# Kernel tuning notes

Hardware: AMD Instinct MI355X
Metric: run time of the kernel (lower is better)

Reference implementation:

```python
import jax, jax.numpy as jnp
import numpy as np

NUM_HEADS = 16
HEAD_DIM = 64
WINDOW = 512
D_MODEL = NUM_HEADS * HEAD_DIM
BATCH = 2
SEQ = 2048


def setup_inputs() -> dict:
    key = jax.random.key(0)
    k1, k2, k3 = jax.random.split(key, 3)
    x = jax.random.normal(k1, (BATCH, SEQ, D_MODEL), dtype=jnp.float32)
    # Dense layer params (lecun_normal-like scale for stability)
    qkv_kernel = jax.random.normal(k2, (D_MODEL, 3 * NUM_HEADS * HEAD_DIM), dtype=jnp.float32) / np.sqrt(D_MODEL)
    qkv_bias = jnp.zeros((3 * NUM_HEADS * HEAD_DIM,), dtype=jnp.float32)
    out_kernel = jax.random.normal(k3, (NUM_HEADS * HEAD_DIM, D_MODEL), dtype=jnp.float32) / np.sqrt(D_MODEL)
    out_bias = jnp.zeros((D_MODEL,), dtype=jnp.float32)
    return {"x": x, "qkv_kernel": qkv_kernel, "qkv_bias": qkv_bias,
            "out_kernel": out_kernel, "out_bias": out_bias}


def reference(x, qkv_kernel, qkv_bias, out_kernel, out_bias):
    b, s, d = x.shape
    qkv = x @ qkv_kernel + qkv_bias                       # (b, s, 3*H*hd)
    qkv = qkv.reshape(b, s, 3, NUM_HEADS, HEAD_DIM)
    q = qkv[:, :, 0].transpose(0, 2, 1, 3)                # (b, H, s, hd)
    k = qkv[:, :, 1].transpose(0, 2, 1, 3)
    v = qkv[:, :, 2].transpose(0, 2, 1, 3)
    scale = 1.0 / jnp.sqrt(jnp.float32(HEAD_DIM)).astype(x.dtype)
    scores = jnp.einsum('bhqd,bhkd->bhqk', q, k) * scale  # (b, H, s, s)
    rows = jnp.arange(s)[:, None]
    cols = jnp.arange(s)[None, :]
    window_mask = (rows - cols >= 0) & (rows - cols < WINDOW)
    scores = jnp.where(window_mask[None, None], scores, jnp.asarray(-1e9, scores.dtype))
    attn = jax.nn.softmax(scores, axis=-1)
    out = jnp.einsum('bhqk,bhkd->bhqd', attn, v)          # (b, H, s, hd)
    out = out.transpose(0, 2, 1, 3).reshape(b, s, -1)
    return out @ out_kernel + out_bias
```

## Files before the change

kernel.cpp:

```cpp
#include <hip/hip_runtime.h>
#include <cstdint>
#include <cstddef>

#define NUM_HEADS 16
#define HEAD_DIM  64
#define WINDOW    512
#define D_MODEL   1024
#define BATCH     2
#define SEQ       2048
#define MTOT      (BATCH*SEQ)
#define NQKV      (3*D_MODEL)

typedef short bf16x8 __attribute__((ext_vector_type(8)));
typedef float f32x4  __attribute__((ext_vector_type(4)));

__device__ __forceinline__ f32x4 mfma16(bf16x8 a, bf16x8 b, f32x4 c) {
  return __builtin_amdgcn_mfma_f32_16x16x32_bf16(a, b, c, 0, 0, 0);
}

__device__ __forceinline__ unsigned short f2bf(float f) {
  unsigned int u = __float_as_uint(f);
  u += 0x7fffu + ((u >> 16) & 1u);
  return (unsigned short)(u >> 16);
}
__device__ __forceinline__ float bf2f(unsigned short b) {
  return __uint_as_float(((unsigned int)b) << 16);
}

__device__ __forceinline__ void gld16(const unsigned short* g, unsigned short* l) {
  __builtin_amdgcn_global_load_lds(
      (const __attribute__((address_space(1))) unsigned int*)g,
      (__attribute__((address_space(3))) unsigned int*)l, 16, 0, 0);
}

__global__ __launch_bounds__(256) void prep_kernel(const float* __restrict__ x,
                                                   const float* __restrict__ qkv_w,
                                                   const float* __restrict__ out_w,
                                                   unsigned short* __restrict__ Xb,
                                                   unsigned short* __restrict__ Wq,
                                                   unsigned short* __restrict__ Wo) {
  __shared__ float tile[32][33];
  const int bid = blockIdx.x, t = threadIdx.x;
  if (bid < 4096) {
    int i = (bid * 256 + t) * 4;
    float4 v = *(const float4*)(x + i);
    ushort4 o;
    o.x = f2bf(v.x); o.y = f2bf(v.y); o.z = f2bf(v.z); o.w = f2bf(v.w);
    *(ushort4*)(Xb + i) = o;
    return;
  }
  const float* in; unsigned short* out; int R, C, bx, by;
  if (bid < 7168) { int b2 = bid - 4096; in = qkv_w; out = Wq; R = D_MODEL; C = NQKV; bx = b2 % 96; by = b2 / 96; }
  else            { int b2 = bid - 7168; in = out_w; out = Wo; R = D_MODEL; C = D_MODEL; bx = b2 & 31; by = b2 >> 5; }
  int tx = t & 31, ty = t >> 5;
  int c0 = bx * 32, r0 = by * 32;
#pragma unroll
  for (int i = 0; i < 32; i += 8)
    tile[ty + i][tx] = in[(size_t)(r0 + ty + i) * C + c0 + tx];
  __syncthreads();
#pragma unroll
  for (int i = 0; i < 32; i += 8)
    out[(size_t)(c0 + ty + i) * R + r0 + tx] = f2bf(tile[tx][ty + i]);
}

template<int TI, bool SWAP, int K>
__device__ __forceinline__ void gemm_mainloop_p3(const unsigned short* __restrict__ A,
                                                 const unsigned short* __restrict__ Bt,
                                                 int m0, int n0,
                                                 unsigned short* sA, unsigned short* sB,
                                                 f32x4 (&acc)[TI][4]) {
  const int t = threadIdx.x;
  const int lane = t & 63, wave = t >> 6;
  const int wm = wave >> 1, wn = wave & 1;
  const int lhi = lane >> 4, llo = lane & 15;
  f32x4 zero = {0.f, 0.f, 0.f, 0.f};
#pragma unroll
  for (int i = 0; i < TI; ++i)
#pragma unroll
    for (int j = 0; j < 4; ++j) acc[i][j] = zero;

  const int cswz = (((t & 3) ^ ((t >> 3) & 3)) << 3);
  const unsigned short* gA = A  + (size_t)(m0 + (t >> 2)) * K + cswz;
  const unsigned short* gB = Bt + (size_t)(n0 + (t >> 2)) * K + cswz;
  const size_t rowskip = (size_t)64 * K;
  const int ldsT = t * 8;
  const int rsw  = (lhi ^ ((llo >> 1) & 3)) * 8;
  const int aoff = (wm * (TI * 16) + llo) * 32 + rsw;
  const int boff = (wn * 64 + llo) * 32 + rsw;
  constexpr int ABUF = TI * 1024;
  constexpr int nIter = K / 32;

  auto stage = [&](int it2) {
    unsigned short* dA = sA + (it2 % 3) * ABUF;
    unsigned short* dB = sB + (it2 % 3) * 4096;
    const int kk = it2 * 32;
    gld16(gA + kk, dA + ldsT);
    if (TI == 4) gld16(gA + kk + rowskip, dA + ldsT + 2048);
    gld16(gB + kk, dB + ldsT);
    gld16(gB + kk + rowskip, dB + ldsT + 2048);
  };

  stage(0);
  stage(1);
#pragma unroll
  for (int it = 0; it < nIter; ++it) {
    if (it + 1 < nIter) {
      if (TI == 4) asm volatile("s_waitcnt vmcnt(4)\n\ts_barrier" ::: "memory");
      else         asm volatile("s_waitcnt vmcnt(3)\n\ts_barrier" ::: "memory");
    } else {
      asm volatile("s_waitcnt vmcnt(0)\n\ts_barrier" ::: "memory");
    }
    if (it + 2 < nIter) stage(it + 2);
    const unsigned short* cA = sA + (it % 3) * ABUF;
    const unsigned short* cB = sB + (it % 3) * 4096;
    bf16x8 af[TI], bfr[4];
#pragma unroll
    for (int i = 0; i < TI; ++i) af[i]  = *(const bf16x8*)(cA + aoff + i * 512);
#pragma unroll
    for (int j = 0; j < 4; ++j)  bfr[j] = *(const bf16x8*)(cB + boff + j * 512);
#pragma unroll
    for (int i = 0; i < TI; ++i)
#pragma unroll
      for (int j = 0; j < 4; ++j)
        acc[i][j] = SWAP ? mfma16(bfr[j], af[i], acc[i][j])
                         : mfma16(af[i], bfr[j], acc[i][j]);
  }
}

__global__ __launch_bounds__(256) void qkv_gemm_kernel(const unsigned short* __restrict__ Xb,
                                                       const unsigned short* __restrict__ Wt,
                                                       const float* __restrict__ bias,
                                                       unsigned short* __restrict__ Qw,
                                                       unsigned short* __restrict__ Kw,
                                                       unsigned short* __restrict__ Vtw) {
  __shared__ __align__(16) unsigned short sA[3][128 * 32];
  __shared__ __align__(16) unsigned short sB[3][128 * 32];
  f32x4 acc[4][4];
  const int m0 = blockIdx.y * 128, n0 = blockIdx.x * 128;
  const int t = threadIdx.x, lane = t & 63, wave = t >> 6;
  const int wm = wave >> 1, wn = wave & 1, lhi = lane >> 4, llo = lane & 15;

  if (n0 < 2048) {
    gemm_mainloop_p3<4, false, D_MODEL>(Xb, Wt, m0, n0, sA[0], sB[0], acc);
    const int c = n0 >> 10;
    unsigned short* __restrict__ Dst = (c == 0) ? Qw : Kw;
    const float qscale = (c == 0) ? 0.125f : 1.0f;
#pragma unroll
    for (int ti = 0; ti < 4; ++ti) {
#pragma unroll
      for (int tj = 0; tj < 4; ++tj) {
        int n = n0 + wn * 64 + tj * 16 + llo;
        float bv = bias[n];
        int h = (n >> 6) & 15, d = n & 63;
#pragma unroll
        for (int r = 0; r < 4; ++r) {
          int m = m0 + wm * 64 + ti * 16 + lhi * 4 + r;
          int b = m >> 11, s = m & 2047;
          int bh = b * 16 + h;
          Dst[((size_t)(bh * 2048 + s)) * 64 + d] = f2bf((acc[ti][tj][r] + bv) * qscale);
        }
      }
    }
  } else {
    gemm_mainloop_p3<4, true, D_MODEL>(Xb, Wt, m0, n0, sA[0], sB[0], acc);
#pragma unroll
    for (int ti = 0; ti < 4; ++ti) {
      int m = m0 + wm * 64 + ti * 16 + llo;
      int b = m >> 11, s = m & 2047;
#pragma unroll
      for (int tj = 0; tj < 4; ++tj) {
        int nb = n0 + wn * 64 + tj * 16 + lhi * 4;
        float4 bv = *(const float4*)(bias + nb);
        int h = (nb >> 6) & 15, dbase = nb & 63;
        int bh = b * 16 + h;
        float bvr[4] = {bv.x, bv.y, bv.z, bv.w};
#pragma unroll
        for (int r = 0; r < 4; ++r)
          Vtw[(size_t)(bh * 64 + dbase + r) * 2048 + s] = f2bf(acc[ti][tj][r] + bvr[r]);
      }
    }
  }
}

__global__ __launch_bounds__(512) void attn_kernel(const unsigned short* __restrict__ Qw,
                                                   const unsigned short* __restrict__ Kw,
                                                   const unsigned short* __restrict__ Vtw,
                                                   unsigned short* __restrict__ AO) {
  __shared__ __align__(16) unsigned short sK[3][64 * 64];
  __shared__ __align__(16) unsigned short sV[3][64 * 64];
  __shared__ __align__(16) unsigned short sP[8][16 * 72];
  const int t = threadIdx.x, lane = t & 63, wave = t >> 6;
  const int lhi = lane >> 4, llo = lane & 15;
  const int bh = blockIdx.x;
  const int q0 = (15 - blockIdx.y) << 7;
  const unsigned short* Qb = Qw  + (size_t)bh * 2048 * 64;
  const unsigned short* Kb = Kw  + (size_t)bh * 2048 * 64;
  const unsigned short* Vb = Vtw + (size_t)bh * 64 * 2048;

  const int qw = q0 + wave * 16;
  const int qrow = qw + llo;
  bf16x8 qf0 = *(const bf16x8*)(Qb + (size_t)qrow * 64 + lhi * 8);
  bf16x8 qf1 = *(const bf16x8*)(Qb + (size_t)qrow * 64 + 32 + lhi * 8);

  const int srow = t >> 3;
  const int scol = ((t & 7) ^ (srow & 7)) * 8;
  const int cpos  = (lhi ^ (llo & 7)) * 8;
  const int cposx = cpos ^ 32;

  float m_i = -1e30f, l_i = 0.f;
  f32x4 o[4];
  f32x4 zero = {0.f, 0.f, 0.f, 0.f};
#pragma unroll
  for (int td = 0; td < 4; ++td) o[td] = zero;

  const int kt_lo = (q0 > 511) ? ((q0 - 511) >> 6) : 0;
  const int kt_hi = (q0 + 127) >> 6;

  auto stageKV = [&](int j) {
    const int k0 = j << 6;
    unsigned short* dK = sK[j % 3];
    unsigned short* dV = sV[j % 3];
    gld16(Kb + (size_t)(k0 + srow) * 64 + scol, dK + t * 8);
    gld16(Vb + (size_t)srow * 2048 + k0 + scol, dV + t * 8);
  };

  stageKV(kt_lo);
  stageKV(kt_lo + 1);

  for (int kt = kt_lo; kt <= kt_hi; ++kt) {
    if (kt < kt_hi) asm volatile("s_waitcnt vmcnt(2)\n\ts_barrier" ::: "memory");
    else            asm volatile("s_waitcnt vmcnt(0)\n\ts_barrier" ::: "memory");
    if (kt + 2 <= kt_hi) stageKV(kt + 2);
    const int k0 = kt << 6;
    if (k0 > qw + 15 || k0 + 63 < qw - (WINDOW - 1)) continue;

    const unsigned short* bK = sK[kt % 3];
    const unsigned short* bV = sV[kt % 3];

    f32x4 st[4];
#pragma unroll
    for (int tk = 0; tk < 4; ++tk) {
      const unsigned short* kr = bK + (tk * 16 + llo) * 64;
      bf16x8 kf0 = *(const bf16x8*)(kr + cpos);
      bf16x8 kf1 = *(const bf16x8*)(kr + cposx);
      f32x4 z = zero;
      z = mfma16(kf0, qf0, z);
      z = mfma16(kf1, qf1, z);
      st[tk] = z;
    }

    const int kb = k0 + lhi * 4;
    float mx = -1e30f;
#pragma unroll
    for (int tk = 0; tk < 4; ++tk)
#pragma unroll
      for (int r = 0; r < 4; ++r) {
        int key = kb + tk * 16 + r;
        bool ok = (key <= qrow) && (qrow - key < WINDOW);
        float s = ok ? st[tk][r] : -1e30f;
        st[tk][r] = s;
        mx = fmaxf(mx, s);
      }
    mx = fmaxf(mx, __shfl_xor(mx, 16));
    mx = fmaxf(mx, __shfl_xor(mx, 32));
    float mn = fmaxf(m_i, mx);
    float a  = __expf(m_i - mn);
    float rs = 0.f;
    unsigned short* pw = &sP[wave][llo * 72];
#pragma unroll
    for (int tk = 0; tk < 4; ++tk) {
      ushort4 pb;
      pb.x = f2bf(__expf(st[tk][0] - mn));
      pb.y = f2bf(__expf(st[tk][1] - mn));
      pb.z = f2bf(__expf(st[tk][2] - mn));
      pb.w = f2bf(__expf(st[tk][3] - mn));
      *(ushort4*)(pw + tk * 16 + lhi * 4) = pb;
      rs += bf2f(pb.x) + bf2f(pb.y) + bf2f(pb.z) + bf2f(pb.w);
    }
    rs += __shfl_xor(rs, 16);
    rs += __shfl_xor(rs, 32);
    l_i = l_i * a + rs;
    m_i = mn;

    float aR[4];
#pragma unroll
    for (int r = 0; r < 4; ++r) aR[r] = __shfl(a, lhi * 4 + r);
#pragma unroll
    for (int td = 0; td < 4; ++td)
#pragma unroll
      for (int r = 0; r < 4; ++r) o[td][r] *= aR[r];

    bf16x8 pf0 = *(const bf16x8*)(pw + lhi * 8);
    bf16x8 pf1 = *(const bf16x8*)(pw + 32 + lhi * 8);
#pragma unroll
    for (int td = 0; td < 4; ++td) {
      const unsigned short* vr = bV + (td * 16 + llo) * 64;
      bf16x8 vf0 = *(const bf16x8*)(vr + cpos);
      bf16x8 vf1 = *(const bf16x8*)(vr + cposx);
      o[td] = mfma16(pf0, vf0, o[td]);
      o[td] = mfma16(pf1, vf1, o[td]);
    }
  }

  float lR[4];
#pragma unroll
  for (int r = 0; r < 4; ++r) lR[r] = 1.f / __shfl(l_i, lhi * 4 + r);
  const int b = bh >> 4, h = bh & 15;
#pragma unroll
  for (int td = 0; td < 4; ++td)
#pragma unroll
    for (int r = 0; r < 4; ++r) {
      int qr = q0 + wave * 16 + lhi * 4 + r;
      AO[(size_t)(b * 2048 + qr) * 1024 + h * 64 + td * 16 + llo] = f2bf(o[td][r] * lR[r]);
    }
}

__global__ __launch_bounds__(256) void out_gemm_kernel(const unsigned short* __restrict__ AO,
                                                       const unsigned short* __restrict__ Wt,
                                                       const float* __restrict__ bias,
                                                       float* __restrict__ out) {
  __shared__ __align__(16) unsigned short sA[3][128 * 32];
  __shared__ __align__(16) unsigned short sB[3][128 * 32];
  f32x4 acc[4][4];
  const int m0 = blockIdx.y * 128, n0 = blockIdx.x * 128;
  gemm_mainloop_p3<4, false, D_MODEL>(AO, Wt, m0, n0, sA[0], sB[0], acc);

  const int t = threadIdx.x, lane = t & 63, wave = t >> 6;
  const int wm = wave >> 1, wn = wave & 1, lhi = lane >> 4, llo = lane & 15;
#pragma unroll
  for (int ti = 0; ti < 4; ++ti)
#pragma unroll
    for (int tj = 0; tj < 4; ++tj) {
      int n = n0 + wn * 64 + tj * 16 + llo;
      float bv = bias[n];
#pragma unroll
      for (int r = 0; r < 4; ++r) {
        int m = m0 + wm * 64 + ti * 16 + lhi * 4 + r;
        out[(size_t)m * D_MODEL + n] = acc[ti][tj][r] + bv;
      }
    }
}

extern "C" void kernel_launch(void* const* d_in, const int* in_sizes, int n_in,
                              void* d_out, int out_size, void* d_ws, size_t ws_size,
                              hipStream_t stream) {
  const float* x      = (const float*)d_in[0];
  const float* qkv_w  = (const float*)d_in[1];
  const float* qkv_b  = (const float*)d_in[2];
  const float* out_w  = (const float*)d_in[3];
  const float* out_b  = (const float*)d_in[4];
  float* out = (float*)d_out;
  char* ws = (char*)d_ws;

  unsigned short* Xb  = (unsigned short*)(ws);
  unsigned short* Wq  = (unsigned short*)(ws + ((size_t)8  << 20));
  unsigned short* Wo  = (unsigned short*)(ws + ((size_t)14 << 20));
  unsigned short* Qw  = (unsigned short*)(ws + ((size_t)16 << 20));
  unsigned short* Kw  = (unsigned short*)(ws + ((size_t)24 << 20));
  unsigned short* Vtw = (unsigned short*)(ws + ((size_t)32 << 20));
  unsigned short* AO  = (unsigned short*)(ws + ((size_t)40 << 20));

  prep_kernel<<<8192, 256, 0, stream>>>(x, qkv_w, out_w, Xb, Wq, Wo);
  qkv_gemm_kernel<<<dim3(NQKV / 128, MTOT / 128), 256, 0, stream>>>(Xb, Wq, qkv_b, Qw, Kw, Vtw);
  attn_kernel<<<dim3(BATCH * NUM_HEADS, SEQ / 128), 512, 0, stream>>>(Qw, Kw, Vtw, AO);
  out_gemm_kernel<<<dim3(D_MODEL / 128, MTOT / 128), 256, 0, stream>>>(AO, Wo, out_b, out);
}
```

Before: 169.8 us.

## Use 512-thread GEMM blocks with 8 waves and skip masking on interior attention tiles

Both GEMM kernels now run 512 threads (8 waves) per 128x128 tile. Each wave computes a 32x64 sub-tile, which halves the accumulator registers and lets every thread issue one load per operand per stage. This is meant to raise occupancy and latency hiding, at the cost of fewer MFMAs per LDS fragment load. The attention kernel also gains a fast path that skips per-element window-mask checks when a key tile lies entirely inside the window for all rows of the wave.

```diff
diff --git a/kernel.cpp b/kernel.cpp
--- a/kernel.cpp
+++ b/kernel.cpp
@@ -63,63 +63,54 @@
     out[(size_t)(c0 + ty + i) * R + r0 + tx] = f2bf(tile[tx][ty + i]);
 }
 
-template<int TI, bool SWAP, int K>
-__device__ __forceinline__ void gemm_mainloop_p3(const unsigned short* __restrict__ A,
+template<bool SWAP, int K>
+__device__ __forceinline__ void gemm_mainloop512(const unsigned short* __restrict__ A,
                                                  const unsigned short* __restrict__ Bt,
                                                  int m0, int n0,
                                                  unsigned short* sA, unsigned short* sB,
-                                                 f32x4 (&acc)[TI][4]) {
+                                                 f32x4 (&acc)[2][4]) {
   const int t = threadIdx.x;
   const int lane = t & 63, wave = t >> 6;
-  const int wm = wave >> 1, wn = wave & 1;
+  const int wr = wave >> 1, wc = wave & 1;
   const int lhi = lane >> 4, llo = lane & 15;
   f32x4 zero = {0.f, 0.f, 0.f, 0.f};
 #pragma unroll
-  for (int i = 0; i < TI; ++i)
+  for (int i = 0; i < 2; ++i)
 #pragma unroll
     for (int j = 0; j < 4; ++j) acc[i][j] = zero;
 
   const int cswz = (((t & 3) ^ ((t >> 3) & 3)) << 3);
   const unsigned short* gA = A  + (size_t)(m0 + (t >> 2)) * K + cswz;
   const unsigned short* gB = Bt + (size_t)(n0 + (t >> 2)) * K + cswz;
-  const size_t rowskip = (size_t)64 * K;
   const int ldsT = t * 8;
   const int rsw  = (lhi ^ ((llo >> 1) & 3)) * 8;
-  const int aoff = (wm * (TI * 16) + llo) * 32 + rsw;
-  const int boff = (wn * 64 + llo) * 32 + rsw;
-  constexpr int ABUF = TI * 1024;
+  const int aoff = (wr * 32 + llo) * 32 + rsw;
+  const int boff = (wc * 64 + llo) * 32 + rsw;
   constexpr int nIter = K / 32;
 
-  auto stage = [&](int it2) {
-    unsigned short* dA = sA + (it2 % 3) * ABUF;
-    unsigned short* dB = sB + (it2 % 3) * 4096;
-    const int kk = it2 * 32;
-    gld16(gA + kk, dA + ldsT);
-    if (TI == 4) gld16(gA + kk + rowskip, dA + ldsT + 2048);
-    gld16(gB + kk, dB + ldsT);
-    gld16(gB + kk + rowskip, dB + ldsT + 2048);
+  auto stage = [&](int s) {
+    unsigned short* dA = sA + (s % 3) * 4096;
+    unsigned short* dB = sB + (s % 3) * 4096;
+    gld16(gA + s * 32, dA + ldsT);
+    gld16(gB + s * 32, dB + ldsT);
   };
 
   stage(0);
   stage(1);
 #pragma unroll
   for (int it = 0; it < nIter; ++it) {
-    if (it + 1 < nIter) {
-      if (TI == 4) asm volatile("s_waitcnt vmcnt(4)\n\ts_barrier" ::: "memory");
-      else         asm volatile("s_waitcnt vmcnt(3)\n\ts_barrier" ::: "memory");
-    } else {
-      asm volatile("s_waitcnt vmcnt(0)\n\ts_barrier" ::: "memory");
-    }
+    if (it + 1 < nIter) asm volatile("s_waitcnt vmcnt(2)\n\ts_barrier" ::: "memory");
+    else                asm volatile("s_waitcnt vmcnt(0)\n\ts_barrier" ::: "memory");
     if (it + 2 < nIter) stage(it + 2);
-    const unsigned short* cA = sA + (it % 3) * ABUF;
+    const unsigned short* cA = sA + (it % 3) * 4096;
     const unsigned short* cB = sB + (it % 3) * 4096;
-    bf16x8 af[TI], bfr[4];
-#pragma unroll
-    for (int i = 0; i < TI; ++i) af[i]  = *(const bf16x8*)(cA + aoff + i * 512);
+    bf16x8 af[2], bfr[4];
+#pragma unroll
+    for (int i = 0; i < 2; ++i) af[i]  = *(const bf16x8*)(cA + aoff + i * 512);
 #pragma unroll
     for (int j = 0; j < 4; ++j)  bfr[j] = *(const bf16x8*)(cB + boff + j * 512);
 #pragma unroll
-    for (int i = 0; i < TI; ++i)
+    for (int i = 0; i < 2; ++i)
 #pragma unroll
       for (int j = 0; j < 4; ++j)
         acc[i][j] = SWAP ? mfma16(bfr[j], af[i], acc[i][j])
@@ -127,49 +118,49 @@
   }
 }
 
-__global__ __launch_bounds__(256) void qkv_gemm_kernel(const unsigned short* __restrict__ Xb,
-                                                       const unsigned short* __restrict__ Wt,
-                                                       const float* __restrict__ bias,
-                                                       unsigned short* __restrict__ Qw,
-                                                       unsigned short* __restrict__ Kw,
-                                                       unsigned short* __restrict__ Vtw) {
+__global__ __launch_bounds__(512, 6) void qkv_gemm_kernel(const unsigned short* __restrict__ Xb,
+                                                          const unsigned short* __restrict__ Wt,
+                                                          const float* __restrict__ bias,
+                                                          unsigned short* __restrict__ Qw,
+                                                          unsigned short* __restrict__ Kw,
+                                                          unsigned short* __restrict__ Vtw) {
   __shared__ __align__(16) unsigned short sA[3][128 * 32];
   __shared__ __align__(16) unsigned short sB[3][128 * 32];
-  f32x4 acc[4][4];
+  f32x4 acc[2][4];
   const int m0 = blockIdx.y * 128, n0 = blockIdx.x * 128;
   const int t = threadIdx.x, lane = t & 63, wave = t >> 6;
-  const int wm = wave >> 1, wn = wave & 1, lhi = lane >> 4, llo = lane & 15;
+  const int wr = wave >> 1, wc = wave & 1, lhi = lane >> 4, llo = lane & 15;
 
   if (n0 < 2048) {
-    gemm_mainloop_p3<4, false, D_MODEL>(Xb, Wt, m0, n0, sA[0], sB[0], acc);
+    gemm_mainloop512<false, D_MODEL>(Xb, Wt, m0, n0, sA[0], sB[0], acc);
     const int c = n0 >> 10;
     unsigned short* __restrict__ Dst = (c == 0) ? Qw : Kw;
-    const float qscale = (c == 0) ? 0.125f : 1.0f;
-#pragma unroll
-    for (int ti = 0; ti < 4; ++ti) {
+    const float qs = (c == 0) ? 0.125f : 1.0f;
+#pragma unroll
+    for (int ti = 0; ti < 2; ++ti) {
 #pragma unroll
       for (int tj = 0; tj < 4; ++tj) {
-        int n = n0 + wn * 64 + tj * 16 + llo;
+        int n = n0 + wc * 64 + tj * 16 + llo;
         float bv = bias[n];
         int h = (n >> 6) & 15, d = n & 63;
 #pragma unroll
         for (int r = 0; r < 4; ++r) {
-          int m = m0 + wm * 64 + ti * 16 + lhi * 4 + r;
+          int m = m0 + wr * 32 + ti * 16 + lhi * 4 + r;
           int b = m >> 11, s = m & 2047;
           int bh = b * 16 + h;
-          Dst[((size_t)(bh * 2048 + s)) * 64 + d] = f2bf((acc[ti][tj][r] + bv) * qscale);
+          Dst[((size_t)(bh * 2048 + s)) * 64 + d] = f2bf((acc[ti][tj][r] + bv) * qs);
         }
       }
     }
   } else {
-    gemm_mainloop_p3<4, true, D_MODEL>(Xb, Wt, m0, n0, sA[0], sB[0], acc);
-#pragma unroll
-    for (int ti = 0; ti < 4; ++ti) {
-      int m = m0 + wm * 64 + ti * 16 + llo;
+    gemm_mainloop512<true, D_MODEL>(Xb, Wt, m0, n0, sA[0], sB[0], acc);
+#pragma unroll
+    for (int ti = 0; ti < 2; ++ti) {
+      int m = m0 + wr * 32 + ti * 16 + llo;
       int b = m >> 11, s = m & 2047;
 #pragma unroll
       for (int tj = 0; tj < 4; ++tj) {
-        int nb = n0 + wn * 64 + tj * 16 + lhi * 4;
+        int nb = n0 + wc * 64 + tj * 16 + lhi * 4;
         float4 bv = *(const float4*)(bias + nb);
         int h = (nb >> 6) & 15, dbase = nb & 63;
         int bh = b * 16 + h;
@@ -249,18 +240,26 @@
       st[tk] = z;
     }
 
+    const bool interior = (k0 >= qw - (WINDOW - 1 - 15)) && (k0 + 63 <= qw);
     const int kb = k0 + lhi * 4;
     float mx = -1e30f;
-#pragma unroll
-    for (int tk = 0; tk < 4; ++tk)
-#pragma unroll
-      for (int r = 0; r < 4; ++r) {
-        int key = kb + tk * 16 + r;
-        bool ok = (key <= qrow) && (qrow - key < WINDOW);
-        float s = ok ? st[tk][r] : -1e30f;
-        st[tk][r] = s;
-        mx = fmaxf(mx, s);
-      }
+    if (interior) {
+#pragma unroll
+      for (int tk = 0; tk < 4; ++tk)
+#pragma unroll
+        for (int r = 0; r < 4; ++r) mx = fmaxf(mx, st[tk][r]);
+    } else {
+#pragma unroll
+      for (int tk = 0; tk < 4; ++tk)
+#pragma unroll
+        for (int r = 0; r < 4; ++r) {
+          int key = kb + tk * 16 + r;
+          bool ok = (key <= qrow) && (qrow - key < WINDOW);
+          float s = ok ? st[tk][r] : -1e30f;
+          st[tk][r] = s;
+          mx = fmaxf(mx, s);
+        }
+    }
     mx = fmaxf(mx, __shfl_xor(mx, 16));
     mx = fmaxf(mx, __shfl_xor(mx, 32));
     float mn = fmaxf(m_i, mx);
@@ -315,27 +314,27 @@
     }
 }
 
-__global__ __launch_bounds__(256) void out_gemm_kernel(const unsigned short* __restrict__ AO,
-                                                       const unsigned short* __restrict__ Wt,
-                                                       const float* __restrict__ bias,
-                                                       float* __restrict__ out) {
+__global__ __launch_bounds__(512, 2) void out_gemm_kernel(const unsigned short* __restrict__ AO,
+                                                          const unsigned short* __restrict__ Wt,
+                                                          const float* __restrict__ bias,
+                                                          float* __restrict__ out) {
   __shared__ __align__(16) unsigned short sA[3][128 * 32];
   __shared__ __align__(16) unsigned short sB[3][128 * 32];
-  f32x4 acc[4][4];
+  f32x4 acc[2][4];
   const int m0 = blockIdx.y * 128, n0 = blockIdx.x * 128;
-  gemm_mainloop_p3<4, false, D_MODEL>(AO, Wt, m0, n0, sA[0], sB[0], acc);
+  gemm_mainloop512<false, D_MODEL>(AO, Wt, m0, n0, sA[0], sB[0], acc);
 
   const int t = threadIdx.x, lane = t & 63, wave = t >> 6;
-  const int wm = wave >> 1, wn = wave & 1, lhi = lane >> 4, llo = lane & 15;
-#pragma unroll
-  for (int ti = 0; ti < 4; ++ti)
+  const int wr = wave >> 1, wc = wave & 1, lhi = lane >> 4, llo = lane & 15;
+#pragma unroll
+  for (int ti = 0; ti < 2; ++ti)
 #pragma unroll
     for (int tj = 0; tj < 4; ++tj) {
-      int n = n0 + wn * 64 + tj * 16 + llo;
+      int n = n0 + wc * 64 + tj * 16 + llo;
       float bv = bias[n];
 #pragma unroll
       for (int r = 0; r < 4; ++r) {
-        int m = m0 + wm * 64 + ti * 16 + lhi * 4 + r;
+        int m = m0 + wr * 32 + ti * 16 + lhi * 4 + r;
         out[(size_t)m * D_MODEL + n] = acc[ti][tj][r] + bv;
       }
     }
@@ -361,7 +360,7 @@
   unsigned short* AO  = (unsigned short*)(ws + ((size_t)40 << 20));
 
   prep_kernel<<<8192, 256, 0, stream>>>(x, qkv_w, out_w, Xb, Wq, Wo);
-  qkv_gemm_kernel<<<dim3(NQKV / 128, MTOT / 128), 256, 0, stream>>>(Xb, Wq, qkv_b, Qw, Kw, Vtw);
+  qkv_gemm_kernel<<<dim3(NQKV / 128, MTOT / 128), 512, 0, stream>>>(Xb, Wq, qkv_b, Qw, Kw, Vtw);
   attn_kernel<<<dim3(BATCH * NUM_HEADS, SEQ / 128), 512, 0, stream>>>(Qw, Kw, Vtw, AO);
-  out_gemm_kernel<<<dim3(D_MODEL / 128, MTOT / 128), 256, 0, stream>>>(AO, Wo, out_b, out);
-}
+  out_gemm_kernel<<<dim3(D_MODEL / 128, MTOT / 128), 512, 0, stream>>>(AO, Wo, out_b, out);
+}
```

Result: faster. 163.8 us (-3.5%).
